# Kernel optimization log

Hardware: AMD Instinct MI355X
Metric: run time of the kernel (lower is better)

## Reference

```python
import jax, jax.numpy as jnp
import numpy as np

N, E, D, L, BOT = 50000, 800000, 64, 5, 15
EPS = 1e-5  # BatchNorm eps (torch default)
GATE = 0.01


def _bn(x, g, b):
    # training-mode BatchNorm1d over the node (batch) axis, biased variance
    m = jnp.mean(x, axis=0)
    v = jnp.mean((x - m) ** 2, axis=0)
    return (x - m) * jax.lax.rsqrt(v + EPS) * g + b


def _adapter(x, w1, b1, w2, b2, g, b):
    # Linear(D->BOT) -> ReLU -> Linear(BOT->D) -> BatchNorm1d
    h = jax.nn.relu(x @ w1 + b1)
    return _bn(h @ w2 + b2, g, b)


def setup_inputs() -> dict:
    key = jax.random.key(0)
    ks = jax.random.split(key, 8)
    x = jax.random.normal(ks[0], (N, D), dtype=jnp.float32)
    edge_index = jax.random.randint(ks[1], (2, E), 0, N, dtype=jnp.int32)
    # per-layer conv Linear weights
    W = jax.random.normal(ks[2], (L, D, D), dtype=jnp.float32) * 0.05
    b = jnp.zeros((L, D), dtype=jnp.float32)
    # per-layer output BatchNorm
    bn_g = jnp.ones((L, D), dtype=jnp.float32)
    bn_b = jnp.zeros((L, D), dtype=jnp.float32)
    # adapter branches: [prompt_num=2, L, ...] (random init so grads are nontrivial)
    pw1 = jax.random.normal(ks[3], (2, L, D, BOT), dtype=jnp.float32) * 0.1
    pb1 = jnp.zeros((2, L, BOT), dtype=jnp.float32)
    pw2 = jax.random.normal(ks[4], (2, L, BOT, D), dtype=jnp.float32) * 0.1
    pb2 = jnp.zeros((2, L, D), dtype=jnp.float32)
    pbn_g = jnp.ones((2, L, D), dtype=jnp.float32)
    pbn_b = jnp.zeros((2, L, D), dtype=jnp.float32)
    gating = jnp.full((2, L, 1), GATE, dtype=jnp.float32)
    return dict(x=x, edge_index=edge_index, W=W, b=b, bn_g=bn_g, bn_b=bn_b,
                pw1=pw1, pb1=pb1, pw2=pw2, pb2=pb2, pbn_g=pbn_g, pbn_b=pbn_b,
                gating=gating)


def reference(x, edge_index, W, b, bn_g, bn_b, pw1, pb1, pw2, pb2, pbn_g, pbn_b, gating):
    src, dst = edge_index[0], edge_index[1]
    h = x
    for l in range(L):
        # mess: sum-aggregate neighbor features (scatter-add over dst)
        x_aggr = jax.ops.segment_sum(h[src], dst, num_segments=N)  # [N, D]
        # conv: Linear on aggregated messages
        h_mlp = x_aggr @ W[l] + b[l]
        hn = _bn(h_mlp, bn_g[l], bn_b[l])
        # adapter branch 0 on layer input, branch 1 on aggregated messages
        hn = hn + _adapter(h, pw1[0, l], pb1[0, l], pw2[0, l], pb2[0, l], pbn_g[0, l], pbn_b[0, l]) * gating[0, l]
        hn = hn + _adapter(x_aggr, pw1[1, l], pb1[1, l], pw2[1, l], pb2[1, l], pbn_g[1, l], pbn_b[1, l]) * gating[1, l]
        if l < L - 1:
            hn = jax.nn.relu(hn)
        # dropout with drop_ratio=0 is a no-op
        h = hn
    return h
```

## Files before the change

kernel.cpp:

```cpp
#include <hip/hip_runtime.h>

#define DIM 64
#define BOT 15
#define NLAYERS 5
#define BN_EPS 1e-5f
#define ROWS 64
#define ROWS_FB 32

__device__ inline void fma4(float4& acc, const float4& a, float s) {
    acc.x = fmaf(a.x, s, acc.x); acc.y = fmaf(a.y, s, acc.y);
    acc.z = fmaf(a.z, s, acc.z); acc.w = fmaf(a.w, s, acc.w);
}
__device__ inline void add4(float4& acc, const float4& a) {
    acc.x += a.x; acc.y += a.y; acc.z += a.z; acc.w += a.w;
}
__device__ inline void fma4sq(float4& acc, const float4& a) {
    acc.x = fmaf(a.x, a.x, acc.x); acc.y = fmaf(a.y, a.y, acc.y);
    acc.z = fmaf(a.z, a.z, acc.z); acc.w = fmaf(a.w, a.w, acc.w);
}
__device__ inline void wavered4(float4& v) {
    v.x += __shfl_xor(v.x, 16); v.y += __shfl_xor(v.y, 16);
    v.z += __shfl_xor(v.z, 16); v.w += __shfl_xor(v.w, 16);
    v.x += __shfl_xor(v.x, 32); v.y += __shfl_xor(v.y, 32);
    v.z += __shfl_xor(v.z, 32); v.w += __shfl_xor(v.w, 32);
}


__global__ __launch_bounds__(256) void hist_k(const int* __restrict__ dst,
                                              int* __restrict__ deg, int E) {
    int e = blockIdx.x * blockDim.x + threadIdx.x;
    if (e < E) atomicAdd(&deg[dst[e]], 1);
}

__global__ __launch_bounds__(1024) void scan_part_k(const int* __restrict__ deg,
                                                    int* __restrict__ excl,
                                                    int* __restrict__ bsum, int n) {
    __shared__ int buf[1024];
    int t = threadIdx.x;
    int idx = blockIdx.x * 1024 + t;
    int v = (idx < n) ? deg[idx] : 0;
    buf[t] = v;
    __syncthreads();
    for (int off = 1; off < 1024; off <<= 1) {
        int x = (t >= off) ? buf[t - off] : 0;
        __syncthreads();
        buf[t] += x;
        __syncthreads();
    }
    if (idx < n) excl[idx] = buf[t] - v;
    if (t == 0) bsum[blockIdx.x] = buf[1023];
}

__global__ __launch_bounds__(1024) void scan_top_k(const int* __restrict__ bsum,
                                                   int* __restrict__ boff, int nb,
                                                   int* __restrict__ row_ptr, int n) {
    __shared__ int buf[1024];
    int t = threadIdx.x;
    int v = (t < nb) ? bsum[t] : 0;
    buf[t] = v;
    __syncthreads();
    for (int off = 1; off < 1024; off <<= 1) {
        int x = (t >= off) ? buf[t - off] : 0;
        __syncthreads();
        buf[t] += x;
        __syncthreads();
    }
    if (t < nb) boff[t] = buf[t] - v;
    if (t == 1023) row_ptr[n] = buf[1023];
}

__global__ __launch_bounds__(256) void scan_add_k(int* __restrict__ row_ptr,
                                                  const int* __restrict__ boff,
                                                  int* __restrict__ deg, int n) {
    int i = blockIdx.x * blockDim.x + threadIdx.x;
    if (i < n) {
        int v = row_ptr[i] + boff[i >> 10];
        row_ptr[i] = v;
        deg[i] = v;
    }
}

__global__ __launch_bounds__(256) void scatter_k(const int* __restrict__ src,
                                                 const int* __restrict__ dst,
                                                 int* __restrict__ cursor,
                                                 int* __restrict__ csr, int E) {
    int e = blockIdx.x * blockDim.x + threadIdx.x;
    if (e < E) {
        int p = atomicAdd(&cursor[dst[e]], 1);
        csr[p] = src[e];
    }
}


__global__ __launch_bounds__(256) void aggr_k(const float* __restrict__ h,
                                              const int* __restrict__ row_ptr,
                                              const int* __restrict__ csr,
                                              float* __restrict__ out, int n) {
    int gid = blockIdx.x * blockDim.x + threadIdx.x;
    int node = gid >> 6;
    int lane = threadIdx.x & 63;
    if (node >= n) return;
    int j = lane >> 4, q = lane & 15;
    int s = row_ptr[node], e = row_ptr[node + 1];
    float4 acc = {0.f, 0.f, 0.f, 0.f};
    #pragma unroll 4
    for (int i = s; i < e; i += 4) {
        int ii = i + j;
        if (ii < e) {
            int idx = csr[ii];
            float4 v = *(const float4*)&h[(size_t)idx * DIM + q * 4];
            add4(acc, v);
        }
    }
    wavered4(acc);
    if (lane < 16) *(float4*)&out[(size_t)node * DIM + q * 4] = acc;
}


__global__ __launch_bounds__(512, 4) void stats_k(
    const float* __restrict__ h, const float* __restrict__ aggr,
    const float* __restrict__ Wc, const float* __restrict__ bc,
    const float* __restrict__ p1a, const float* __restrict__ b1a,
    const float* __restrict__ p2a, const float* __restrict__ b2a,
    const float* __restrict__ p1b, const float* __restrict__ b1b,
    const float* __restrict__ p2b, const float* __restrict__ b2b,
    float* __restrict__ partials,
    float* __restrict__ yv, float* __restrict__ uv, float* __restrict__ vv,
    int n) {
    __shared__ float xa_s[ROWS][68];
    __shared__ float wc_s[64][64];
    __shared__ float p1t_s[2][15][68];
    __shared__ float p2_s[2][15][64];
    __shared__ float m_s[2][ROWS][17];
    __shared__ float red_s[6][8][64];

    int t = threadIdx.x;
    int rowBase = blockIdx.x * ROWS;

    #pragma unroll
    for (int i = 0; i < 2; i++) {
        int idx = t + i * 512;
        int r = idx >> 4, c4 = (idx & 15) * 4;
        int gr = rowBase + r;
        float4 va = {0.f, 0.f, 0.f, 0.f};
        if (gr < n) va = *(const float4*)&aggr[(size_t)gr * DIM + c4];
        *(float4*)&xa_s[r][c4] = va;
    }
    #pragma unroll
    for (int i = 0; i < 2; i++) {
        int idx = t + i * 512;
        int k = idx >> 4, c4 = (idx & 15) * 4;
        *(float4*)&wc_s[k][c4] = *(const float4*)&Wc[k * DIM + c4];
    }
    if (t < 240) {
        int m = t >> 4, c4 = (t & 15) * 4;
        *(float4*)&p2_s[0][m][c4] = *(const float4*)&p2a[m * DIM + c4];
        *(float4*)&p2_s[1][m][c4] = *(const float4*)&p2b[m * DIM + c4];
    }
    #pragma unroll
    for (int i = 0; i < 2; i++) {
        int idx = t + i * 512;
        if (idx < 960) {
            int k = idx / 15, m = idx % 15;
            p1t_s[0][m][k] = p1a[idx];
            p1t_s[1][m][k] = p1b[idx];
        }
    }
    __syncthreads();

    {
        int m = t & 15, r2 = t >> 4;
        if (m < 15) {
            #pragma unroll
            for (int half = 0; half < 2; half++) {
                int r = r2 + half * 32;
                int gr = rowBase + r;
                if (gr < n) {
                    float sA = b1a[m], sB = b1b[m];
                    const float4* hp = (const float4*)&h[(size_t)gr * DIM];
                    #pragma unroll 4
                    for (int kq = 0; kq < 16; kq++) {
                        float4 hv = hp[kq];
                        float4 av = *(const float4*)&xa_s[r][kq * 4];
                        float4 wA = *(const float4*)&p1t_s[0][m][kq * 4];
                        float4 wB = *(const float4*)&p1t_s[1][m][kq * 4];
                        sA = fmaf(hv.x, wA.x, sA); sA = fmaf(hv.y, wA.y, sA);
                        sA = fmaf(hv.z, wA.z, sA); sA = fmaf(hv.w, wA.w, sA);
                        sB = fmaf(av.x, wB.x, sB); sB = fmaf(av.y, wB.y, sB);
                        sB = fmaf(av.z, wB.z, sB); sB = fmaf(av.w, wB.w, sB);
                    }
                    m_s[0][r][m] = fmaxf(sA, 0.f);
                    m_s[1][r][m] = fmaxf(sB, 0.f);
                } else {
                    m_s[0][r][m] = 0.f;
                    m_s[1][r][m] = 0.f;
                }
            }
        }
    }
    __syncthreads();

    int cg = t & 15, rg = t >> 4;
    int c0 = cg * 4;
    int r0 = rg, r1 = rg + 32;

    float4 s0 = *(const float4*)&bc[c0];
    float4 s1 = s0;
    #pragma unroll 4
    for (int kq = 0; kq < 16; kq++) {
        float4 w0 = *(const float4*)&wc_s[kq * 4 + 0][c0];
        float4 w1 = *(const float4*)&wc_s[kq * 4 + 1][c0];
        float4 w2 = *(const float4*)&wc_s[kq * 4 + 2][c0];
        float4 w3 = *(const float4*)&wc_s[kq * 4 + 3][c0];
        float4 a0 = *(const float4*)&xa_s[r0][kq * 4];
        float4 a1 = *(const float4*)&xa_s[r1][kq * 4];
        fma4(s0, w0, a0.x); fma4(s0, w1, a0.y); fma4(s0, w2, a0.z); fma4(s0, w3, a0.w);
        fma4(s1, w0, a1.x); fma4(s1, w1, a1.y); fma4(s1, w2, a1.z); fma4(s1, w3, a1.w);
    }

    float4 u0 = *(const float4*)&b2a[c0];
    float4 u1 = u0;
    float4 v0 = *(const float4*)&b2b[c0];
    float4 v1 = v0;
    #pragma unroll 5
    for (int m = 0; m < BOT; m++) {
        float4 wa = *(const float4*)&p2_s[0][m][c0];
        float4 wb = *(const float4*)&p2_s[1][m][c0];
        float a0 = m_s[0][r0][m], a1 = m_s[0][r1][m];
        float b0 = m_s[1][r0][m], b1 = m_s[1][r1][m];
        fma4(u0, wa, a0); fma4(u1, wa, a1);
        fma4(v0, wb, b0); fma4(v1, wb, b1);
    }

    float4 sy = {0,0,0,0}, sy2 = {0,0,0,0};
    float4 su = {0,0,0,0}, su2 = {0,0,0,0};
    float4 sv = {0,0,0,0}, sv2 = {0,0,0,0};
    {
        int gr = rowBase + r0;
        if (gr < n) {
            size_t o = (size_t)gr * DIM + c0;
            *(float4*)&yv[o] = s0; *(float4*)&uv[o] = u0; *(float4*)&vv[o] = v0;
            add4(sy, s0); fma4sq(sy2, s0);
            add4(su, u0); fma4sq(su2, u0);
            add4(sv, v0); fma4sq(sv2, v0);
        }
        gr = rowBase + r1;
        if (gr < n) {
            size_t o = (size_t)gr * DIM + c0;
            *(float4*)&yv[o] = s1; *(float4*)&uv[o] = u1; *(float4*)&vv[o] = v1;
            add4(sy, s1); fma4sq(sy2, s1);
            add4(su, u1); fma4sq(su2, u1);
            add4(sv, v1); fma4sq(sv2, v1);
        }
    }

    wavered4(sy); wavered4(sy2);
    wavered4(su); wavered4(su2);
    wavered4(sv); wavered4(sv2);

    int wv = t >> 6, lane = t & 63;
    if (lane < 16) {
        *(float4*)&red_s[0][wv][c0] = sy;
        *(float4*)&red_s[1][wv][c0] = sy2;
        *(float4*)&red_s[2][wv][c0] = su;
        *(float4*)&red_s[3][wv][c0] = su2;
        *(float4*)&red_s[4][wv][c0] = sv;
        *(float4*)&red_s[5][wv][c0] = sv2;
    }
    __syncthreads();
    if (t < DIM) {
        #pragma unroll
        for (int j = 0; j < 6; j++) {
            float v = red_s[j][0][t] + red_s[j][1][t] + red_s[j][2][t] + red_s[j][3][t]
                    + red_s[j][4][t] + red_s[j][5][t] + red_s[j][6][t] + red_s[j][7][t];
            partials[((size_t)blockIdx.x * 6 + j) * DIM + t] = v;
        }
    }
}


template <int RELU>
__global__ __launch_bounds__(256) void apply_k(
    const float* __restrict__ yv, const float* __restrict__ uv,
    const float* __restrict__ vv, const float* __restrict__ ST,
    float* __restrict__ out, int n4) {
    int i = blockIdx.x * blockDim.x + threadIdx.x;
    if (i >= n4) return;
    int c4 = (i & 15) * 4;
    float4 S0 = *(const float4*)&ST[c4];
    float4 T0 = *(const float4*)&ST[64 + c4];
    float4 S1 = *(const float4*)&ST[128 + c4];
    float4 T1 = *(const float4*)&ST[192 + c4];
    float4 S2 = *(const float4*)&ST[256 + c4];
    float4 T2 = *(const float4*)&ST[320 + c4];
    float4 y = *(const float4*)&yv[(size_t)i * 4];
    float4 u = *(const float4*)&uv[(size_t)i * 4];
    float4 v = *(const float4*)&vv[(size_t)i * 4];
    float4 r;
    r.x = fmaf(y.x, S0.x, T0.x) + fmaf(u.x, S1.x, T1.x) + fmaf(v.x, S2.x, T2.x);
    r.y = fmaf(y.y, S0.y, T0.y) + fmaf(u.y, S1.y, T1.y) + fmaf(v.y, S2.y, T2.y);
    r.z = fmaf(y.z, S0.z, T0.z) + fmaf(u.z, S1.z, T1.z) + fmaf(v.z, S2.z, T2.z);
    r.w = fmaf(y.w, S0.w, T0.w) + fmaf(u.w, S1.w, T1.w) + fmaf(v.w, S2.w, T2.w);
    if (RELU) {
        r.x = fmaxf(r.x, 0.f); r.y = fmaxf(r.y, 0.f);
        r.z = fmaxf(r.z, 0.f); r.w = fmaxf(r.w, 0.f);
    }
    *(float4*)&out[(size_t)i * 4] = r;
}


template <int MODE>
__global__ __launch_bounds__(256) void layer_k(
    const float* __restrict__ h, const float* __restrict__ aggr,
    const float* __restrict__ Wc, const float* __restrict__ bc,
    const float* __restrict__ p1a, const float* __restrict__ b1a,
    const float* __restrict__ p2a, const float* __restrict__ b2a,
    const float* __restrict__ p1b, const float* __restrict__ b1b,
    const float* __restrict__ p2b, const float* __restrict__ b2b,
    float* __restrict__ partials, const float* __restrict__ ST,
    float* __restrict__ hout, int n) {
    __shared__ float xh[ROWS_FB][DIM + 1];
    __shared__ float xa[ROWS_FB][DIM + 1];
    __shared__ float m0[ROWS_FB][17];
    __shared__ float m1[ROWS_FB][17];
    __shared__ float red[6][4][DIM];

    int t = threadIdx.x;
    int rowBase = blockIdx.x * ROWS_FB;

    #pragma unroll
    for (int i = 0; i < (ROWS_FB * DIM) / 256; i++) {
        int idx = t + i * 256;
        int r = idx >> 6, c = idx & 63;
        int gr = rowBase + r;
        float vh = 0.f, va = 0.f;
        if (gr < n) { vh = h[(size_t)gr * DIM + c]; va = aggr[(size_t)gr * DIM + c]; }
        xh[r][c] = vh;
        xa[r][c] = va;
    }
    __syncthreads();

    {
        int r = t >> 3, sub = t & 7;
        #pragma unroll
        for (int half = 0; half < 2; half++) {
            int m = sub + half * 8;
            if (m < BOT) {
                float s0 = b1a[m], s1 = b1b[m];
                #pragma unroll
                for (int k = 0; k < DIM; k++) {
                    s0 = fmaf(xh[r][k], p1a[k * BOT + m], s0);
                    s1 = fmaf(xa[r][k], p1b[k * BOT + m], s1);
                }
                m0[r][m] = fmaxf(s0, 0.f);
                m1[r][m] = fmaxf(s1, 0.f);
            }
        }
    }
    __syncthreads();

    int col = t & 63;
    int rg = t >> 6;
    float sums[6] = {0.f, 0.f, 0.f, 0.f, 0.f, 0.f};
    float S0 = 0, T0 = 0, S1 = 0, T1 = 0, S2 = 0, T2 = 0;
    if (MODE != 0) {
        S0 = ST[col];        T0 = ST[64 + col];
        S1 = ST[128 + col];  T1 = ST[192 + col];
        S2 = ST[256 + col];  T2 = ST[320 + col];
    }
    #pragma unroll
    for (int i = 0; i < ROWS_FB / 4; i++) {
        int r = rg + i * 4;
        int gr = rowBase + r;
        float s = bc[col];
        #pragma unroll
        for (int k = 0; k < DIM; k++) s = fmaf(xa[r][k], Wc[k * DIM + col], s);
        float u = b2a[col];
        #pragma unroll
        for (int m = 0; m < BOT; m++) u = fmaf(m0[r][m], p2a[m * DIM + col], u);
        float v = b2b[col];
        #pragma unroll
        for (int m = 0; m < BOT; m++) v = fmaf(m1[r][m], p2b[m * DIM + col], v);
        if (MODE == 0) {
            if (gr < n) {
                sums[0] += s; sums[1] += s * s;
                sums[2] += u; sums[3] += u * u;
                sums[4] += v; sums[5] += v * v;
            }
        } else {
            float r0 = fmaf(s, S0, T0) + fmaf(u, S1, T1) + fmaf(v, S2, T2);
            if (MODE == 2) r0 = fmaxf(r0, 0.f);
            if (gr < n) hout[(size_t)gr * DIM + col] = r0;
        }
    }

    if (MODE == 0) {
        #pragma unroll
        for (int j = 0; j < 6; j++) red[j][rg][col] = sums[j];
        __syncthreads();
        if (t < DIM) {
            #pragma unroll
            for (int j = 0; j < 6; j++) {
                float v = red[j][0][t] + red[j][1][t] + red[j][2][t] + red[j][3][t];
                partials[((size_t)blockIdx.x * 6 + j) * DIM + t] = v;
            }
        }
    }
}


__global__ __launch_bounds__(256) void reduce_fold_k(
    const float* __restrict__ partials, int nb, int n,
    const float* __restrict__ bn_g, const float* __restrict__ bn_b,
    const float* __restrict__ pg0, const float* __restrict__ pb0,
    const float* __restrict__ pg1, const float* __restrict__ pb1,
    const float* __restrict__ gating, int l, float* __restrict__ ST) {
    __shared__ double red[6][256];
    int col = blockIdx.x;
    int t = threadIdx.x;
    double acc[6] = {0, 0, 0, 0, 0, 0};
    for (int b = t; b < nb; b += 256) {
        const float* p = partials + (size_t)b * 6 * DIM + col;
        #pragma unroll
        for (int j = 0; j < 6; j++) acc[j] += (double)p[j * DIM];
    }
    #pragma unroll
    for (int j = 0; j < 6; j++) red[j][t] = acc[j];
    __syncthreads();
    for (int off = 128; off > 0; off >>= 1) {
        if (t < off) {
            #pragma unroll
            for (int j = 0; j < 6; j++) red[j][t] += red[j][t + off];
        }
        __syncthreads();
    }
    if (t < 3) {
        int stat = t;
        float mean = (float)(red[2 * stat][0] / (double)n);
        float var = (float)(red[2 * stat + 1][0] / (double)n) - mean * mean;
        float rstd = rsqrtf(fmaxf(var, 0.f) + BN_EPS);
        float g, bb, gate;
        if (stat == 0)      { g = bn_g[col]; bb = bn_b[col]; gate = 1.f; }
        else if (stat == 1) { g = pg0[col];  bb = pb0[col];  gate = gating[0 * NLAYERS + l]; }
        else                { g = pg1[col];  bb = pb1[col];  gate = gating[1 * NLAYERS + l]; }
        float S = g * rstd * gate;
        float T = (bb - mean * g * rstd) * gate;
        ST[stat * 128 + col] = S;
        ST[stat * 128 + 64 + col] = T;
    }
}


static inline char* bump(char*& p, size_t bytes) {
    char* r = p;
    p += (bytes + 255) & ~(size_t)255;
    return r;
}

extern "C" void kernel_launch(void* const* d_in, const int* in_sizes, int n_in,
                              void* d_out, int out_size, void* d_ws, size_t ws_size,
                              hipStream_t stream) {
    const float* x      = (const float*)d_in[0];
    const int*   ei     = (const int*)d_in[1];
    const float* W      = (const float*)d_in[2];
    const float* bconv  = (const float*)d_in[3];
    const float* bn_g   = (const float*)d_in[4];
    const float* bn_b   = (const float*)d_in[5];
    const float* pw1    = (const float*)d_in[6];
    const float* pb1    = (const float*)d_in[7];
    const float* pw2    = (const float*)d_in[8];
    const float* pb2    = (const float*)d_in[9];
    const float* pbn_g  = (const float*)d_in[10];
    const float* pbn_b  = (const float*)d_in[11];
    const float* gating = (const float*)d_in[12];

    int n = in_sizes[0] / DIM;
    int E = in_sizes[1] / 2;
    int nbS  = (n + ROWS - 1) / ROWS;
    int nbFB = (n + ROWS_FB - 1) / ROWS_FB;
    int nb1024 = (n + 1023) / 1024;
    size_t n64b = (size_t)n * DIM * sizeof(float);

    char* p = (char*)d_ws;
    float* h_ws     = (float*)bump(p, n64b);
    float* partials = (float*)bump(p, (size_t)nbFB * 6 * DIM * sizeof(float));
    float* ST       = (float*)bump(p, 6 * 128 * sizeof(float));
    int*   bsum     = (int*)bump(p, (size_t)nb1024 * sizeof(int));
    int*   boff     = (int*)bump(p, (size_t)nb1024 * sizeof(int));
    int*   deg      = (int*)bump(p, (size_t)n * sizeof(int));
    int*   row_ptr  = (int*)bump(p, (size_t)(n + 1) * sizeof(int));
    int*   csr      = (int*)bump(p, (size_t)E * sizeof(int));
    float* aggr     = (float*)bump(p, n64b);
    float* yv = (float*)bump(p, n64b);
    float* uv = (float*)bump(p, n64b);
    float* vv = (float*)bump(p, n64b);
    bool fast = ((size_t)(p - (char*)d_ws) <= ws_size);

    const int* esrc = ei;
    const int* edst = ei + E;

    hipMemsetAsync(deg, 0, (size_t)n * sizeof(int), stream);
    hist_k<<<(E + 255) / 256, 256, 0, stream>>>(edst, deg, E);
    scan_part_k<<<nb1024, 1024, 0, stream>>>(deg, row_ptr, bsum, n);
    scan_top_k<<<1, 1024, 0, stream>>>(bsum, boff, nb1024, row_ptr, n);
    scan_add_k<<<(n + 255) / 256, 256, 0, stream>>>(row_ptr, boff, deg, n);
    scatter_k<<<(E + 255) / 256, 256, 0, stream>>>(esrc, edst, deg, csr, E);

    for (int l = 0; l < NLAYERS; l++) {
        const float* Wl  = W     + (size_t)l * DIM * DIM;
        const float* bl  = bconv + (size_t)l * DIM;
        const float* bgl = bn_g  + (size_t)l * DIM;
        const float* bbl = bn_b  + (size_t)l * DIM;
        const float* p1a = pw1 + ((size_t)0 * NLAYERS + l) * DIM * BOT;
        const float* p1b = pw1 + ((size_t)1 * NLAYERS + l) * DIM * BOT;
        const float* b1a = pb1 + ((size_t)0 * NLAYERS + l) * BOT;
        const float* b1b = pb1 + ((size_t)1 * NLAYERS + l) * BOT;
        const float* p2a = pw2 + ((size_t)0 * NLAYERS + l) * BOT * DIM;
        const float* p2b = pw2 + ((size_t)1 * NLAYERS + l) * BOT * DIM;
        const float* b2a = pb2 + ((size_t)0 * NLAYERS + l) * DIM;
        const float* b2b = pb2 + ((size_t)1 * NLAYERS + l) * DIM;
        const float* g0  = pbn_g + ((size_t)0 * NLAYERS + l) * DIM;
        const float* g1  = pbn_g + ((size_t)1 * NLAYERS + l) * DIM;
        const float* be0 = pbn_b + ((size_t)0 * NLAYERS + l) * DIM;
        const float* be1 = pbn_b + ((size_t)1 * NLAYERS + l) * DIM;

        const float* hin = (l == 0) ? x : h_ws;

        aggr_k<<<(n + 3) / 4, 256, 0, stream>>>(hin, row_ptr, csr, aggr, n);

        if (fast) {
            stats_k<<<nbS, 512, 0, stream>>>(
                hin, aggr, Wl, bl, p1a, b1a, p2a, b2a,
                p1b, b1b, p2b, b2b, partials, yv, uv, vv, n);

            reduce_fold_k<<<DIM, 256, 0, stream>>>(partials, nbS, n, bgl, bbl,
                                                   g0, be0, g1, be1, gating, l, ST);

            int n4 = n * (DIM / 4);
            float* outp = (l < NLAYERS - 1) ? h_ws : (float*)d_out;
            if (l < NLAYERS - 1)
                apply_k<1><<<(n4 + 255) / 256, 256, 0, stream>>>(yv, uv, vv, ST, outp, n4);
            else
                apply_k<0><<<(n4 + 255) / 256, 256, 0, stream>>>(yv, uv, vv, ST, outp, n4);
        } else {
            layer_k<0><<<nbFB, 256, 0, stream>>>(
                hin, aggr, Wl, bl, p1a, b1a, p2a, b2a, p1b, b1b, p2b, b2b,
                partials, nullptr, nullptr, n);

            reduce_fold_k<<<DIM, 256, 0, stream>>>(partials, nbFB, n, bgl, bbl,
                                                   g0, be0, g1, be1, gating, l, ST);

            if (l < NLAYERS - 1) {
                layer_k<2><<<nbFB, 256, 0, stream>>>(
                    hin, aggr, Wl, bl, p1a, b1a, p2a, b2a, p1b, b1b, p2b, b2b,
                    nullptr, ST, h_ws, n);
            } else {
                layer_k<1><<<nbFB, 256, 0, stream>>>(
                    hin, aggr, Wl, bl, p1a, b1a, p2a, b2a, p1b, b1b, p2b, b2b,
                    nullptr, ST, (float*)d_out, n);
            }
        }
    }
}
```

Before: 498.5 us.

## Build CSR via two-pass bucketed partition instead of global random scatter

Replaces the single-pass CSR scatter, which does random global atomics and writes for every edge, with two passes. The first pass partitions edges into 256-node destination buckets using shared-memory histograms and per-bucket cursors. The second pass scatters each bucket locally so its atomics and writes stay within a small address range. This adds a kernel launch and an extra write and read of the edge list through the yv scratch buffer, and assumes at most 256 buckets (n up to 65536).

New measurement: 488.8 us. Within noise of the previous version (-2.0%).

```diff
diff --git a/kernel.cpp b/kernel.cpp
--- a/kernel.cpp
+++ b/kernel.cpp
@@ -6,6 +6,7 @@
 #define BN_EPS 1e-5f
 #define ROWS 64
 #define ROWS_FB 32
+#define BKT_SHIFT 8
 
 __device__ inline void fma4(float4& acc, const float4& a, float s) {
     acc.x = fmaf(a.x, s, acc.x); acc.y = fmaf(a.y, s, acc.y);
@@ -71,12 +72,14 @@
 
 __global__ __launch_bounds__(256) void scan_add_k(int* __restrict__ row_ptr,
                                                   const int* __restrict__ boff,
-                                                  int* __restrict__ deg, int n) {
+                                                  int* __restrict__ deg,
+                                                  int* __restrict__ bcur, int n) {
     int i = blockIdx.x * blockDim.x + threadIdx.x;
     if (i < n) {
         int v = row_ptr[i] + boff[i >> 10];
         row_ptr[i] = v;
         deg[i] = v;
+        if ((i & 255) == 0) bcur[i >> BKT_SHIFT] = v;
     }
 }
 
@@ -88,6 +91,56 @@
     if (e < E) {
         int p = atomicAdd(&cursor[dst[e]], 1);
         csr[p] = src[e];
+    }
+}
+
+__global__ __launch_bounds__(256) void part_k(const int* __restrict__ src,
+                                              const int* __restrict__ dst,
+                                              int* __restrict__ bcur,
+                                              int2* __restrict__ part, int E) {
+    __shared__ int hist[256];
+    __shared__ int cur[256];
+    int t = threadIdx.x;
+    int base = blockIdx.x * 2048;
+    hist[t] = 0;
+    __syncthreads();
+    int2 ed[8];
+    int bk[8];
+    #pragma unroll
+    for (int k = 0; k < 8; k++) {
+        int i = base + k * 256 + t;
+        if (i < E) {
+            ed[k].x = src[i];
+            ed[k].y = dst[i];
+            bk[k] = ed[k].y >> BKT_SHIFT;
+            atomicAdd(&hist[bk[k]], 1);
+        } else bk[k] = -1;
+    }
+    __syncthreads();
+    int h = hist[t];
+    if (h > 0) cur[t] = atomicAdd(&bcur[t], h);
+    __syncthreads();
+    #pragma unroll
+    for (int k = 0; k < 8; k++) {
+        if (bk[k] >= 0) {
+            int p = atomicAdd(&cur[bk[k]], 1);
+            part[p] = ed[k];
+        }
+    }
+}
+
+__global__ __launch_bounds__(256) void bscat_k(const int2* __restrict__ part,
+                                               const int* __restrict__ row_ptr,
+                                               int* __restrict__ cursor,
+                                               int* __restrict__ csr, int n) {
+    int b = blockIdx.x;
+    int lo = row_ptr[b << BKT_SHIFT];
+    int hiN = (b + 1) << BKT_SHIFT;
+    int hi = row_ptr[hiN < n ? hiN : n];
+    for (int i = lo + (int)threadIdx.x; i < hi; i += 256) {
+        int2 e = part[i];
+        int p = atomicAdd(&cursor[e.y], 1);
+        csr[p] = e.x;
     }
 }
 
@@ -479,6 +532,7 @@
     int nbS  = (n + ROWS - 1) / ROWS;
     int nbFB = (n + ROWS_FB - 1) / ROWS_FB;
     int nb1024 = (n + 1023) / 1024;
+    int nbkt = (n + 255) >> BKT_SHIFT;
     size_t n64b = (size_t)n * DIM * sizeof(float);
 
     char* p = (char*)d_ws;
@@ -487,6 +541,7 @@
     float* ST       = (float*)bump(p, 6 * 128 * sizeof(float));
     int*   bsum     = (int*)bump(p, (size_t)nb1024 * sizeof(int));
     int*   boff     = (int*)bump(p, (size_t)nb1024 * sizeof(int));
+    int*   bcur     = (int*)bump(p, 257 * sizeof(int));
     int*   deg      = (int*)bump(p, (size_t)n * sizeof(int));
     int*   row_ptr  = (int*)bump(p, (size_t)(n + 1) * sizeof(int));
     int*   csr      = (int*)bump(p, (size_t)E * sizeof(int));
@@ -495,6 +550,7 @@
     float* uv = (float*)bump(p, n64b);
     float* vv = (float*)bump(p, n64b);
     bool fast = ((size_t)(p - (char*)d_ws) <= ws_size);
+    int2* part = (int2*)yv;
 
     const int* esrc = ei;
     const int* edst = ei + E;
@@ -503,8 +559,13 @@
     hist_k<<<(E + 255) / 256, 256, 0, stream>>>(edst, deg, E);
     scan_part_k<<<nb1024, 1024, 0, stream>>>(deg, row_ptr, bsum, n);
     scan_top_k<<<1, 1024, 0, stream>>>(bsum, boff, nb1024, row_ptr, n);
-    scan_add_k<<<(n + 255) / 256, 256, 0, stream>>>(row_ptr, boff, deg, n);
-    scatter_k<<<(E + 255) / 256, 256, 0, stream>>>(esrc, edst, deg, csr, E);
+    scan_add_k<<<(n + 255) / 256, 256, 0, stream>>>(row_ptr, boff, deg, bcur, n);
+    if (fast) {
+        part_k<<<(E + 2047) / 2048, 256, 0, stream>>>(esrc, edst, bcur, part, E);
+        bscat_k<<<nbkt, 256, 0, stream>>>(part, row_ptr, deg, csr, n);
+    } else {
+        scatter_k<<<(E + 255) / 256, 256, 0, stream>>>(esrc, edst, deg, csr, E);
+    }
 
     for (int l = 0; l < NLAYERS; l++) {
         const float* Wl  = W     + (size_t)l * DIM * DIM;
```
